# Kernel tuning notes

Measured on AMD Instinct MI355X. Metric: run time of the kernel, lower is better.

The kernel has to match this reference:

```python
import jax, jax.numpy as jnp
import numpy as np

N_NODES = 100000
N_EDGES = 1000000
IN_FEATS = 128
HIDDEN = 256


def setup_inputs() -> dict:
    key = jax.random.key(0)
    ks = jax.random.split(key, 8)
    h_src_nodes = jax.random.normal(ks[0], (N_NODES, IN_FEATS), dtype=jnp.float32)
    h_dst_nodes = jax.random.normal(ks[1], (N_NODES, IN_FEATS), dtype=jnp.float32)
    src = jax.random.randint(ks[2], (N_EDGES,), 0, N_NODES, dtype=jnp.int32)
    dst = jax.random.randint(ks[3], (N_EDGES,), 0, N_NODES, dtype=jnp.int32)
    # MLP params, stored as [in, out] so forward is x @ W + b
    s1 = 1.0 / np.sqrt(2 * IN_FEATS)
    s2 = 1.0 / np.sqrt(HIDDEN)
    W1 = jax.random.uniform(ks[4], (2 * IN_FEATS, HIDDEN), jnp.float32, -s1, s1)
    b1 = jax.random.uniform(ks[5], (HIDDEN,), jnp.float32, -s1, s1)
    W2 = jax.random.uniform(ks[6], (HIDDEN, 1), jnp.float32, -s2, s2)
    b2 = jax.random.uniform(ks[7], (1,), jnp.float32, -s2, s2)
    return {"h_src_nodes": h_src_nodes, "h_dst_nodes": h_dst_nodes,
            "src": src, "dst": dst, "W1": W1, "b1": b1, "W2": W2, "b2": b2}


def reference(h_src_nodes, h_dst_nodes, src, dst, W1, b1, W2, b2):
    # gather endpoint features per edge, concat -> [E, 2*in_feats]
    h_cat = jnp.concatenate([h_src_nodes[src], h_dst_nodes[dst]], axis=1)
    hidden = jax.nn.relu(h_cat @ W1 + b1)        # [E, hidden]
    score = (hidden @ W2 + b2).squeeze(-1)        # [E]
    return score
```

## Files before the change

### kernel.cpp

```cpp
#include <hip/hip_runtime.h>
#include <hip/hip_bf16.h>
#include <stdint.h>

#define IN_FEATS 128
#define HID 256

typedef __bf16 bf16x8 __attribute__((ext_vector_type(8)));
typedef float  f32x4  __attribute__((ext_vector_type(4)));

__global__ void k_prep(const float* __restrict__ W1, __bf16* __restrict__ W1T) {
    int k = blockIdx.x;
    int n = threadIdx.x;
    W1T[(size_t)n * (2 * IN_FEATS) + k] = (__bf16)W1[(size_t)k * HID + n];
}

__global__ __launch_bounds__(256) void k_proj(
    const float* __restrict__ hs, const float* __restrict__ hd,
    const __bf16* __restrict__ W1T, const float* __restrict__ b1,
    __bf16* __restrict__ Ps, __bf16* __restrict__ Pd)
{
    const int which = blockIdx.y;
    const float* __restrict__ h = which ? hd : hs;
    __bf16* __restrict__ P = which ? Pd : Ps;
    const int koff = which ? IN_FEATS : 0;

    const int lane = threadIdx.x & 63;
    const int w    = threadIdx.x >> 6;
    const int n0   = w * 64;
    const int node0 = blockIdx.x * 32;
    const int qr = lane & 15;
    const int qg = lane >> 4;

    f32x4 acc[2][4];
#pragma unroll
    for (int m = 0; m < 2; ++m)
#pragma unroll
        for (int n = 0; n < 4; ++n) acc[m][n] = (f32x4){0.f, 0.f, 0.f, 0.f};

#pragma unroll
    for (int ks = 0; ks < 4; ++ks) {
        const int k0 = ks * 32 + qg * 8;
        bf16x8 a[2];
#pragma unroll
        for (int m = 0; m < 2; ++m) {
            const float* ap = h + (size_t)(node0 + m * 16 + qr) * IN_FEATS + k0;
            float4 f0 = *(const float4*)ap;
            float4 f1 = *(const float4*)(ap + 4);
            bf16x8 t;
            t[0] = (__bf16)f0.x; t[1] = (__bf16)f0.y; t[2] = (__bf16)f0.z; t[3] = (__bf16)f0.w;
            t[4] = (__bf16)f1.x; t[5] = (__bf16)f1.y; t[6] = (__bf16)f1.z; t[7] = (__bf16)f1.w;
            a[m] = t;
        }
#pragma unroll
        for (int n = 0; n < 4; ++n) {
            const __bf16* bp = W1T + (size_t)(n0 + n * 16 + qr) * (2 * IN_FEATS) + koff + k0;
            bf16x8 b = *(const bf16x8*)bp;
#pragma unroll
            for (int m = 0; m < 2; ++m)
                acc[m][n] = __builtin_amdgcn_mfma_f32_16x16x32_bf16(a[m], b, acc[m][n], 0, 0, 0);
        }
    }

#pragma unroll
    for (int n = 0; n < 4; ++n) {
        const int col = n0 + n * 16 + qr;
        const float bias = which ? 0.f : b1[col];
#pragma unroll
        for (int m = 0; m < 2; ++m) {
            const int rowb = node0 + m * 16 + qg * 4;
#pragma unroll
            for (int i = 0; i < 4; ++i)
                P[(size_t)(rowb + i) * HID + col] = (__bf16)(acc[m][n][i] + bias);
        }
    }
}

__device__ __forceinline__ float bflo(unsigned u) { return __uint_as_float(u << 16); }
__device__ __forceinline__ float bfhi(unsigned u) { return __uint_as_float(u & 0xffff0000u); }

__device__ __forceinline__ float dot8(uint4 s, uint4 d, float4 w0, float4 w1) {
    float r = 0.f, hv;
    hv = fmaxf(bflo(s.x) + bflo(d.x), 0.f); r = fmaf(hv, w0.x, r);
    hv = fmaxf(bfhi(s.x) + bfhi(d.x), 0.f); r = fmaf(hv, w0.y, r);
    hv = fmaxf(bflo(s.y) + bflo(d.y), 0.f); r = fmaf(hv, w0.z, r);
    hv = fmaxf(bfhi(s.y) + bfhi(d.y), 0.f); r = fmaf(hv, w0.w, r);
    hv = fmaxf(bflo(s.z) + bflo(d.z), 0.f); r = fmaf(hv, w1.x, r);
    hv = fmaxf(bfhi(s.z) + bfhi(d.z), 0.f); r = fmaf(hv, w1.y, r);
    hv = fmaxf(bflo(s.w) + bflo(d.w), 0.f); r = fmaf(hv, w1.z, r);
    hv = fmaxf(bfhi(s.w) + bfhi(d.w), 0.f); r = fmaf(hv, w1.w, r);
    return r;
}

__global__ __launch_bounds__(256) void k_edge(
    const __bf16* __restrict__ Ps, const __bf16* __restrict__ Pd,
    const int* __restrict__ src, const int* __restrict__ dst,
    const float* __restrict__ W2, const float* __restrict__ b2,
    float* __restrict__ out, int E)
{
    const int lane = threadIdx.x & 63;
    const int q = lane & 15;
    const int g = lane >> 4;
    const int wave = blockIdx.x * 4 + (threadIdx.x >> 6);
    const int nw = gridDim.x * 4;

    const float4* W2v = (const float4*)W2;
    const float4 wa0 = W2v[2 * q], wa1 = W2v[2 * q + 1];
    const float4 wb0 = W2v[32 + 2 * q], wb1 = W2v[32 + 2 * q + 1];
    const float bias = b2[0];

    for (int base = wave * 4; base < E; base += nw * 4) {
        const int e = base + g;
        float acc = 0.f;
        const bool valid = (e < E);
        if (valid) {
            const int s = src[e];
            const int d = dst[e];
            const uint4* ps = (const uint4*)(Ps + (size_t)s * HID);
            const uint4* pd = (const uint4*)(Pd + (size_t)d * HID);
            uint4 a0 = ps[q];
            uint4 a1 = ps[16 + q];
            uint4 c0 = pd[q];
            uint4 c1 = pd[16 + q];
            acc  = dot8(a0, c0, wa0, wa1);
            acc += dot8(a1, c1, wb0, wb1);
        }
#pragma unroll
        for (int m = 1; m < 16; m <<= 1) acc += __shfl_xor(acc, m, 64);
        if (q == 0 && valid) out[e] = acc + bias;
    }
}

extern "C" void kernel_launch(void* const* d_in, const int* in_sizes, int n_in,
                              void* d_out, int out_size, void* d_ws, size_t ws_size,
                              hipStream_t stream) {
    const float* h_src = (const float*)d_in[0];
    const float* h_dst = (const float*)d_in[1];
    const int*   src   = (const int*)d_in[2];
    const int*   dst   = (const int*)d_in[3];
    const float* W1    = (const float*)d_in[4];
    const float* b1    = (const float*)d_in[5];
    const float* W2    = (const float*)d_in[6];
    const float* b2    = (const float*)d_in[7];
    float* out = (float*)d_out;

    const int E  = in_sizes[2];
    const int NN = in_sizes[0] / IN_FEATS;

    __bf16* W1T = (__bf16*)d_ws;
    __bf16* Ps  = (__bf16*)((char*)d_ws + (size_t)(2 * IN_FEATS) * HID * sizeof(__bf16));
    __bf16* Pd  = Ps + (size_t)NN * HID;

    k_prep<<<2 * IN_FEATS, HID, 0, stream>>>(W1, W1T);
    dim3 gA(NN / 32, 2);
    k_proj<<<gA, 256, 0, stream>>>(h_src, h_dst, W1T, b1, Ps, Pd);
    k_edge<<<2048, 256, 0, stream>>>(Ps, Pd, src, dst, W2, b2, out, E);
}
```

Baseline: 366.2 us.

## Pre-pack W1 in MFMA fragment order, pack bf16 stores, unroll edge loop by two

The weight prep kernel now writes W1 directly in per-lane MFMA B-fragment order, so the projection kernel reads each fragment as one contiguous 16-byte load per lane instead of strided rows. The projection epilogue exchanges values between adjacent lanes to write pairs of bf16 as 32-bit stores rather than scattered 16-bit stores. The edge kernel processes two edges per 16-lane group per iteration to put more independent gathers in flight. The lane shuffles and the doubled register use are the added costs.

```diff
diff --git a/kernel.cpp b/kernel.cpp
--- a/kernel.cpp
+++ b/kernel.cpp
@@ -8,21 +8,37 @@
 typedef __bf16 bf16x8 __attribute__((ext_vector_type(8)));
 typedef float  f32x4  __attribute__((ext_vector_type(4)));
 
-__global__ void k_prep(const float* __restrict__ W1, __bf16* __restrict__ W1T) {
-    int k = blockIdx.x;
-    int n = threadIdx.x;
-    W1T[(size_t)n * (2 * IN_FEATS) + k] = (__bf16)W1[(size_t)k * HID + n];
+__device__ __forceinline__ unsigned pk2(float a, float b) {
+    __bf16 ba = (__bf16)a, bb = (__bf16)b;
+    unsigned short ua = __builtin_bit_cast(unsigned short, ba);
+    unsigned short ub = __builtin_bit_cast(unsigned short, bb);
+    return (unsigned)ua | ((unsigned)ub << 16);
+}
+
+__global__ void k_prep(const float* __restrict__ W1, __bf16* __restrict__ W1P) {
+    int t = blockIdx.x * blockDim.x + threadIdx.x;
+    int lane  = t & 63;
+    int nblk  = (t >> 6) & 15;
+    int ks    = (t >> 10) & 3;
+    int which = (t >> 12) & 1;
+    int qr = lane & 15, qg = lane >> 4;
+    int n  = nblk * 16 + qr;
+    int k0 = which * 128 + ks * 32 + qg * 8;
+    bf16x8 v;
+#pragma unroll
+    for (int j = 0; j < 8; ++j)
+        v[j] = (__bf16)W1[(size_t)(k0 + j) * HID + n];
+    *(bf16x8*)(W1P + (size_t)t * 8) = v;
 }
 
 __global__ __launch_bounds__(256) void k_proj(
     const float* __restrict__ hs, const float* __restrict__ hd,
-    const __bf16* __restrict__ W1T, const float* __restrict__ b1,
+    const __bf16* __restrict__ W1P, const float* __restrict__ b1,
     __bf16* __restrict__ Ps, __bf16* __restrict__ Pd)
 {
     const int which = blockIdx.y;
     const float* __restrict__ h = which ? hd : hs;
     __bf16* __restrict__ P = which ? Pd : Ps;
-    const int koff = which ? IN_FEATS : 0;
 
     const int lane = threadIdx.x & 63;
     const int w    = threadIdx.x >> 6;
@@ -30,6 +46,7 @@
     const int node0 = blockIdx.x * 32;
     const int qr = lane & 15;
     const int qg = lane >> 4;
+    const bf16x8* __restrict__ W1Pv = (const bf16x8*)W1P;
 
     f32x4 acc[2][4];
 #pragma unroll
@@ -53,14 +70,15 @@
         }
 #pragma unroll
         for (int n = 0; n < 4; ++n) {
-            const __bf16* bp = W1T + (size_t)(n0 + n * 16 + qr) * (2 * IN_FEATS) + koff + k0;
-            bf16x8 b = *(const bf16x8*)bp;
+            bf16x8 b = W1Pv[((size_t)(which * 4 + ks) * 16 + w * 4 + n) * 64 + lane];
 #pragma unroll
             for (int m = 0; m < 2; ++m)
                 acc[m][n] = __builtin_amdgcn_mfma_f32_16x16x32_bf16(a[m], b, acc[m][n], 0, 0, 0);
         }
     }
 
+    const bool even = (qr & 1) == 0;
+    const int i0 = even ? 0 : 2;
 #pragma unroll
     for (int n = 0; n < 4; ++n) {
         const int col = n0 + n * 16 + qr;
@@ -68,9 +86,18 @@
 #pragma unroll
         for (int m = 0; m < 2; ++m) {
             const int rowb = node0 + m * 16 + qg * 4;
+            float v[4], o[4];
 #pragma unroll
-            for (int i = 0; i < 4; ++i)
-                P[(size_t)(rowb + i) * HID + col] = (__bf16)(acc[m][n][i] + bias);
+            for (int i = 0; i < 4; ++i) {
+                v[i] = acc[m][n][i] + bias;
+                o[i] = __shfl_xor(v[i], 1, 64);
+            }
+#pragma unroll
+            for (int i = 0; i < 2; ++i) {
+                const int r = i0 + i;
+                unsigned wd = even ? pk2(v[r], o[r]) : pk2(o[r], v[r]);
+                *(unsigned*)(P + (size_t)(rowb + r) * HID + (col & ~1)) = wd;
+            }
         }
     }
 }
@@ -108,25 +135,37 @@
     const float4 wb0 = W2v[32 + 2 * q], wb1 = W2v[32 + 2 * q + 1];
     const float bias = b2[0];
 
-    for (int base = wave * 4; base < E; base += nw * 4) {
-        const int e = base + g;
-        float acc = 0.f;
-        const bool valid = (e < E);
-        if (valid) {
-            const int s = src[e];
-            const int d = dst[e];
-            const uint4* ps = (const uint4*)(Ps + (size_t)s * HID);
-            const uint4* pd = (const uint4*)(Pd + (size_t)d * HID);
-            uint4 a0 = ps[q];
-            uint4 a1 = ps[16 + q];
-            uint4 c0 = pd[q];
-            uint4 c1 = pd[16 + q];
-            acc  = dot8(a0, c0, wa0, wa1);
-            acc += dot8(a1, c1, wb0, wb1);
+    for (int base = wave * 8; base < E; base += nw * 8) {
+        const int e0 = base + g;
+        const int e1 = base + 4 + g;
+        const bool v0 = (e0 < E), v1 = (e1 < E);
+        float acc0 = 0.f, acc1 = 0.f;
+        if (v0) {
+            const uint4* ps = (const uint4*)(Ps + (size_t)src[e0] * HID);
+            const uint4* pd = (const uint4*)(Pd + (size_t)dst[e0] * HID);
+            uint4 a0 = ps[q], a1 = ps[16 + q], c0 = pd[q], c1 = pd[16 + q];
+            if (v1) {
+                const uint4* ps1 = (const uint4*)(Ps + (size_t)src[e1] * HID);
+                const uint4* pd1 = (const uint4*)(Pd + (size_t)dst[e1] * HID);
+                uint4 b0 = ps1[q], b1v = ps1[16 + q], d0 = pd1[q], d1 = pd1[16 + q];
+                acc0  = dot8(a0, c0, wa0, wa1);
+                acc0 += dot8(a1, c1, wb0, wb1);
+                acc1  = dot8(b0, d0, wa0, wa1);
+                acc1 += dot8(b1v, d1, wb0, wb1);
+            } else {
+                acc0  = dot8(a0, c0, wa0, wa1);
+                acc0 += dot8(a1, c1, wb0, wb1);
+            }
         }
 #pragma unroll
-        for (int m = 1; m < 16; m <<= 1) acc += __shfl_xor(acc, m, 64);
-        if (q == 0 && valid) out[e] = acc + bias;
+        for (int m = 1; m < 16; m <<= 1) {
+            acc0 += __shfl_xor(acc0, m, 64);
+            acc1 += __shfl_xor(acc1, m, 64);
+        }
+        if (q == 0) {
+            if (v0) out[e0] = acc0 + bias;
+            if (v1) out[e1] = acc1 + bias;
+        }
     }
 }
 
@@ -146,12 +185,12 @@
     const int E  = in_sizes[2];
     const int NN = in_sizes[0] / IN_FEATS;
 
-    __bf16* W1T = (__bf16*)d_ws;
+    __bf16* W1P = (__bf16*)d_ws;
     __bf16* Ps  = (__bf16*)((char*)d_ws + (size_t)(2 * IN_FEATS) * HID * sizeof(__bf16));
     __bf16* Pd  = Ps + (size_t)NN * HID;
 
-    k_prep<<<2 * IN_FEATS, HID, 0, stream>>>(W1, W1T);
+    k_prep<<<32, 256, 0, stream>>>(W1, W1P);
     dim3 gA(NN / 32, 2);
-    k_proj<<<gA, 256, 0, stream>>>(h_src, h_dst, W1T, b1, Ps, Pd);
+    k_proj<<<gA, 256, 0, stream>>>(h_src, h_dst, W1P, b1, Ps, Pd);
     k_edge<<<2048, 256, 0, stream>>>(Ps, Pd, src, dst, W2, b2, out, E);
 }
```

New measurement: 338.4 us. -7.6%, faster.
